# Performance work log

Hardware: AMD Instinct MI355X
Metric: run time of the kernel (lower is better)

## Reference

```python
import jax, jax.numpy as jnp
import numpy as np

B, S, E, H = 8, 1024, 1024, 16
D = E // H  # head dimension = 64


def setup_inputs() -> dict:
    key = jax.random.key(0)
    ks = jax.random.split(key, 9)
    sc = 1.0 / np.sqrt(E)
    return {
        "q": jax.random.normal(ks[0], (B, S, E), dtype=jnp.float32),
        "Wq_w": jax.random.normal(ks[1], (E, E), dtype=jnp.float32) * sc,
        "Wq_b": jax.random.normal(ks[2], (E,), dtype=jnp.float32) * 0.01,
        "Wk_w": jax.random.normal(ks[3], (E, E), dtype=jnp.float32) * sc,
        "Wk_b": jax.random.normal(ks[4], (E,), dtype=jnp.float32) * 0.01,
        "Wv_w": jax.random.normal(ks[5], (E, E), dtype=jnp.float32) * sc,
        "Wv_b": jax.random.normal(ks[6], (E,), dtype=jnp.float32) * 0.01,
        "Wo_w": jax.random.normal(ks[7], (E, E), dtype=jnp.float32) * sc,
        "Wo_b": jax.random.normal(ks[8], (E,), dtype=jnp.float32) * 0.01,
    }


def reference(q, Wq_w, Wq_b, Wk_w, Wk_b, Wv_w, Wv_b, Wo_w, Wo_b):
    # Linear projections (torch Linear: x @ W.T + b)
    Q = q @ Wq_w.T + Wq_b
    K = q @ Wk_w.T + Wk_b  # self-attention: k = v = q
    V = q @ Wv_w.T + Wv_b
    # [B, S, E] -> [B, H, S, D]
    Q = Q.reshape(B, S, H, D).transpose(0, 2, 1, 3)
    K = K.reshape(B, S, H, D).transpose(0, 2, 1, 3)
    V = V.reshape(B, S, H, D).transpose(0, 2, 1, 3)
    # Scores [B, H, S, S], scaled by sqrt(head_dim)
    scores = jnp.einsum('bhqd,bhkd->bhqk', Q, K) / jnp.sqrt(jnp.float32(D))
    attn = jax.nn.softmax(scores, axis=-1)
    # dropout p=0.0 (eval mode) -> identity
    out = jnp.einsum('bhqk,bhkd->bhqd', attn, V)
    out = out.transpose(0, 2, 1, 3).reshape(B, S, E)
    out = out @ Wo_w.T + Wo_b
    return out, attn
```

## Files before the change

### kernel.cpp

```cpp
#include <hip/hip_runtime.h>

using bf16x8 = __attribute__((ext_vector_type(8))) __bf16;
using f32x4  = __attribute__((ext_vector_type(4))) float;

#define NE 1024
#define C1E 0.18033688011112042f
#define C2E -11.541560327111707f

__device__ __forceinline__ unsigned short f2b(float f) {
    unsigned u = __builtin_bit_cast(unsigned, f);
    u = (u + 0x7FFFu + ((u >> 16) & 1u)) >> 16;
    return (unsigned short)u;
}

typedef __attribute__((address_space(1))) const void gvoid_t;
typedef __attribute__((address_space(3))) void lvoid_t;

__device__ __forceinline__ void stage128(const unsigned short* gbase, char* lds, int tid)
{
    const int w = tid >> 6, l = tid & 63;
    #pragma unroll
    for (int i = 0; i < 4; ++i) {
        int grp = i * 4 + w;
        int row = grp * 8 + (l >> 3);
        int srcb = ((l & 7) * 16) ^ ((l >> 3) << 4);
        const char* g = (const char*)(gbase + (size_t)row * NE) + srcb;
        char* d = lds + grp * 1024;
        __builtin_amdgcn_global_load_lds((gvoid_t*)g, (lvoid_t*)d, 16, 0, 0);
    }
}

__device__ __forceinline__ void stage64x256(const unsigned short* gbase, char* lds, int tid)
{
    const int w = tid >> 6, l = tid & 63;
    #pragma unroll
    for (int i = 0; i < 4; ++i) {
        int row0 = i * 16 + w * 4;
        int row = row0 + (l >> 4);
        int srcb = ((l & 15) * 16) ^ ((row & 7) << 4);
        const char* g = (const char*)(gbase + (size_t)row * 1024) + srcb;
        char* d = lds + row0 * 256;
        __builtin_amdgcn_global_load_lds((gvoid_t*)g, (lvoid_t*)d, 16, 0, 0);
    }
}

__global__ __launch_bounds__(256)
void conv_bf16(const float* __restrict__ src, unsigned short* __restrict__ dst)
{
    size_t i = ((size_t)blockIdx.x * 256 + threadIdx.x) * 8;
    float4 a0 = *(const float4*)(src + i);
    float4 a1 = *(const float4*)(src + i + 4);
    uint4 p;
    p.x = f2b(a0.x) | ((unsigned)f2b(a0.y) << 16);
    p.y = f2b(a0.z) | ((unsigned)f2b(a0.w) << 16);
    p.z = f2b(a1.x) | ((unsigned)f2b(a1.y) << 16);
    p.w = f2b(a1.z) | ((unsigned)f2b(a1.w) << 16);
    *(uint4*)(dst + i) = p;
}

template<int MODE>
__global__ __launch_bounds__(256)
void proj_bt(const unsigned short* __restrict__ A, const unsigned short* __restrict__ W,
             const float* __restrict__ bias, void* __restrict__ outp)
{
    __shared__ char Asm[16384], Bsm[16384];
    const int tid  = threadIdx.x;
    const int lane = tid & 63;
    const int wid  = tid >> 6;
    const int wr = wid >> 1, wc = wid & 1;
    const int swz = (blockIdx.x & 7) * 64 + (blockIdx.x >> 3);
    const int rowbase = (swz >> 3) * 128;
    const int colbase = (swz & 7) * 128;
    f32x4 acc[4][4] = {};

    for (int kt = 0; kt < 16; ++kt) {
        __syncthreads();
        stage128(A + (size_t)rowbase * NE + kt * 64, Asm, tid);
        stage128(W + (size_t)colbase * NE + kt * 64, Bsm, tid);
        __syncthreads();
        #pragma unroll
        for (int ks = 0; ks < 2; ++ks) {
            const int kb = ks * 64 + (lane >> 4) * 16;
            bf16x8 af[4], bf[4];
            #pragma unroll
            for (int m = 0; m < 4; ++m) {
                int row = wr * 64 + m * 16 + (lane & 15);
                af[m] = *(const bf16x8*)(Asm + ((row * 128 + kb) ^ ((row & 7) << 4)));
            }
            #pragma unroll
            for (int n = 0; n < 4; ++n) {
                int row = wc * 64 + n * 16 + (lane & 15);
                bf[n] = *(const bf16x8*)(Bsm + ((row * 128 + kb) ^ ((row & 7) << 4)));
            }
            #pragma unroll
            for (int m = 0; m < 4; ++m)
                #pragma unroll
                for (int n = 0; n < 4; ++n)
                    acc[m][n] = __builtin_amdgcn_mfma_f32_16x16x32_bf16(af[m], bf[n], acc[m][n], 0, 0, 0);
        }
    }

    #pragma unroll
    for (int m = 0; m < 4; ++m) {
        #pragma unroll
        for (int n = 0; n < 4; ++n) {
            int col = colbase + wc * 64 + n * 16 + (lane & 15);
            float bv = bias[col];
            #pragma unroll
            for (int r = 0; r < 4; ++r) {
                int row = rowbase + wr * 64 + m * 16 + (lane >> 4) * 4 + r;
                float v = acc[m][n][r] + bv;
                if (MODE == 0) {
                    ((unsigned short*)outp)[(size_t)row * NE + col] = f2b(v);
                } else if (MODE == 1) {
                    int b = row >> 10, s = row & 1023, h = col >> 6, d = col & 63;
                    ((unsigned short*)outp)[((size_t)((b * 16 + h) * 64 + d) << 10) + s] = f2b(v);
                } else {
                    ((float*)outp)[(size_t)row * NE + col] = v;
                }
            }
        }
    }
}

__global__ __launch_bounds__(256, 2)
void fused_attn(const unsigned short* __restrict__ Q,
                const unsigned short* __restrict__ K,
                const unsigned short* __restrict__ VT,
                float* __restrict__ attn, unsigned short* __restrict__ Og)
{
    __shared__ char Ksm[16384];
    __shared__ char Vsm[16384];
    __shared__ char Psm[32768];
    __shared__ float rs4[4][128];
    __shared__ float lt[128];
    const int tid  = threadIdx.x;
    const int lane = tid & 63;
    const int w    = tid >> 6;
    const int swzb = (blockIdx.x & 7) * 128 + (blockIdx.x >> 3);
    const int bh = swzb >> 3, qt = swzb & 7;
    const int b = bh >> 4, h = bh & 15;
    const unsigned short* Qg = Q  + (size_t)(b * 1024 + qt * 128) * 1024 + h * 64;
    const unsigned short* Kg = K  + (size_t)(b * 1024) * 1024 + h * 64;
    const unsigned short* Vg = VT + (size_t)bh * 64 * 1024;

    stage128(Qg, Psm, tid);
    __syncthreads();
    bf16x8 qf[2][8];
    #pragma unroll
    for (int ks = 0; ks < 2; ++ks) {
        const int kb = ks * 64 + (lane >> 4) * 16;
        #pragma unroll
        for (int n = 0; n < 8; ++n) {
            int row = n * 16 + (lane & 15);
            qf[ks][n] = *(const bf16x8*)(Psm + ((row * 128 + kb) ^ ((row & 7) << 4)));
        }
    }
    stage128(Kg, Ksm, tid);

    float rs_p[8] = {0.f, 0.f, 0.f, 0.f, 0.f, 0.f, 0.f, 0.f};
    for (int kt = 0; kt < 8; ++kt) {
        __syncthreads();
        f32x4 sa[2][8] = {};
        __builtin_amdgcn_s_setprio(1);
        #pragma unroll
        for (int ks = 0; ks < 2; ++ks) {
            const int kb = ks * 64 + (lane >> 4) * 16;
            bf16x8 kf[2];
            #pragma unroll
            for (int m = 0; m < 2; ++m) {
                int row = w * 32 + m * 16 + (lane & 15);
                kf[m] = *(const bf16x8*)(Ksm + ((row * 128 + kb) ^ ((row & 7) << 4)));
            }
            #pragma unroll
            for (int m = 0; m < 2; ++m)
                #pragma unroll
                for (int n = 0; n < 8; ++n)
                    sa[m][n] = __builtin_amdgcn_mfma_f32_16x16x32_bf16(kf[m], qf[ks][n], sa[m][n], 0, 0, 0);
        }
        __builtin_amdgcn_s_setprio(0);
        __syncthreads();
        if (kt < 7) stage128(Kg + (size_t)((kt + 1) * 128) * 1024, Ksm, tid);
        #pragma unroll
        for (int n = 0; n < 8; ++n)
            #pragma unroll
            for (int m = 0; m < 2; ++m)
                #pragma unroll
                for (int r = 0; r < 4; ++r)
                    rs_p[n] += exp2f(fmaf(sa[m][n][r], C1E, C2E));
    }
    #pragma unroll
    for (int n = 0; n < 8; ++n) {
        rs_p[n] += __shfl_xor(rs_p[n], 16);
        rs_p[n] += __shfl_xor(rs_p[n], 32);
    }
    if (lane < 16) {
        #pragma unroll
        for (int n = 0; n < 8; ++n) rs4[w][n * 16 + lane] = rs_p[n];
    }
    __syncthreads();
    if (tid < 128) {
        float l = rs4[0][tid] + rs4[1][tid] + rs4[2][tid] + rs4[3][tid];
        lt[tid] = C2E - __log2f(l);
    }
    stage128(Kg, Ksm, tid);

    f32x4 oa[2][4] = {};
    float* attnq = attn + ((size_t)bh * 1024 + qt * 128) * 1024;
    for (int kt = 0; kt < 8; ++kt) {
        __syncthreads();
        stage64x256(Vg + kt * 128, Vsm, tid);
        f32x4 sa[2][8] = {};
        __builtin_amdgcn_s_setprio(1);
        #pragma unroll
        for (int ks = 0; ks < 2; ++ks) {
            const int kb = ks * 64 + (lane >> 4) * 16;
            bf16x8 kf[2];
            #pragma unroll
            for (int m = 0; m < 2; ++m) {
                int row = w * 32 + m * 16 + (lane & 15);
                kf[m] = *(const bf16x8*)(Ksm + ((row * 128 + kb) ^ ((row & 7) << 4)));
            }
            #pragma unroll
            for (int m = 0; m < 2; ++m)
                #pragma unroll
                for (int n = 0; n < 8; ++n)
                    sa[m][n] = __builtin_amdgcn_mfma_f32_16x16x32_bf16(kf[m], qf[ks][n], sa[m][n], 0, 0, 0);
        }
        __builtin_amdgcn_s_setprio(0);
        #pragma unroll
        for (int n = 0; n < 8; ++n) {
            int q = n * 16 + (lane & 15);
            float ltq = lt[q];
            #pragma unroll
            for (int m = 0; m < 2; ++m) {
                int k0 = w * 32 + m * 16 + (lane >> 4) * 4;
                float4 p4;
                p4.x = exp2f(fmaf(sa[m][n][0], C1E, ltq));
                p4.y = exp2f(fmaf(sa[m][n][1], C1E, ltq));
                p4.z = exp2f(fmaf(sa[m][n][2], C1E, ltq));
                p4.w = exp2f(fmaf(sa[m][n][3], C1E, ltq));
                *(float4*)(attnq + (size_t)q * 1024 + kt * 128 + k0) = p4;
                uint2 pk;
                pk.x = f2b(p4.x) | ((unsigned)f2b(p4.y) << 16);
                pk.y = f2b(p4.z) | ((unsigned)f2b(p4.w) << 16);
                *(uint2*)(Psm + ((q * 256 + k0 * 2) ^ ((q & 7) << 4))) = pk;
            }
        }
        __syncthreads();
        if (kt < 7) stage128(Kg + (size_t)((kt + 1) * 128) * 1024, Ksm, tid);
        __builtin_amdgcn_s_setprio(1);
        #pragma unroll
        for (int ks = 0; ks < 4; ++ks) {
            const int kb = ks * 64 + (lane >> 4) * 16;
            bf16x8 pa[2], vb[4];
            #pragma unroll
            for (int m2 = 0; m2 < 2; ++m2) {
                int row = w * 32 + m2 * 16 + (lane & 15);
                pa[m2] = *(const bf16x8*)(Psm + ((row * 256 + kb) ^ ((row & 7) << 4)));
            }
            #pragma unroll
            for (int n2 = 0; n2 < 4; ++n2) {
                int d = n2 * 16 + (lane & 15);
                vb[n2] = *(const bf16x8*)(Vsm + d * 256 + (kb ^ ((d & 7) << 4)));
            }
            #pragma unroll
            for (int m2 = 0; m2 < 2; ++m2)
                #pragma unroll
                for (int n2 = 0; n2 < 4; ++n2)
                    oa[m2][n2] = __builtin_amdgcn_mfma_f32_16x16x32_bf16(pa[m2], vb[n2], oa[m2][n2], 0, 0, 0);
        }
        __builtin_amdgcn_s_setprio(0);
    }
    unsigned short* Ob = Og + (size_t)(b * 1024 + qt * 128) * 1024 + h * 64;
    #pragma unroll
    for (int m2 = 0; m2 < 2; ++m2)
        #pragma unroll
        for (int n2 = 0; n2 < 4; ++n2) {
            int d = n2 * 16 + (lane & 15);
            #pragma unroll
            for (int r = 0; r < 4; ++r) {
                int qrow = w * 32 + m2 * 16 + (lane >> 4) * 4 + r;
                Ob[(size_t)qrow * 1024 + d] = f2b(oa[m2][n2][r]);
            }
        }
}

extern "C" void kernel_launch(void* const* d_in, const int* in_sizes, int n_in,
                              void* d_out, int out_size, void* d_ws, size_t ws_size,
                              hipStream_t stream) {
    (void)in_sizes; (void)n_in; (void)out_size; (void)ws_size;
    const float* q    = (const float*)d_in[0];
    const float* Wq_w = (const float*)d_in[1];
    const float* Wq_b = (const float*)d_in[2];
    const float* Wk_w = (const float*)d_in[3];
    const float* Wk_b = (const float*)d_in[4];
    const float* Wv_w = (const float*)d_in[5];
    const float* Wv_b = (const float*)d_in[6];
    const float* Wo_w = (const float*)d_in[7];
    const float* Wo_b = (const float*)d_in[8];

    char* ws = (char*)d_ws;
    unsigned short* Qws  = (unsigned short*)(ws);
    unsigned short* Kws  = (unsigned short*)(ws + (16u << 20));
    unsigned short* VTws = (unsigned short*)(ws + (32u << 20));

    float* outp  = (float*)d_out;
    float* attnp = outp + 8388608;

    char* scr = (char*)attnp;
    unsigned short* qbf = (unsigned short*)scr;
    unsigned short* wqb = (unsigned short*)(scr + (16u << 20));
    unsigned short* wkb = (unsigned short*)(scr + (18u << 20));
    unsigned short* wvb = (unsigned short*)(scr + (20u << 20));

    dim3 blk(256);
    conv_bf16<<<dim3(4096), blk, 0, stream>>>(q, qbf);
    conv_bf16<<<dim3(512),  blk, 0, stream>>>(Wq_w, wqb);
    conv_bf16<<<dim3(512),  blk, 0, stream>>>(Wk_w, wkb);
    conv_bf16<<<dim3(512),  blk, 0, stream>>>(Wv_w, wvb);
    proj_bt<0><<<dim3(512), blk, 0, stream>>>(qbf, wqb, Wq_b, Qws);
    proj_bt<0><<<dim3(512), blk, 0, stream>>>(qbf, wkb, Wk_b, Kws);
    proj_bt<1><<<dim3(512), blk, 0, stream>>>(qbf, wvb, Wv_b, VTws);
    fused_attn<<<dim3(1024), blk, 0, stream>>>(Qws, Kws, VTws, attnp, Qws);
    conv_bf16<<<dim3(512),  blk, 0, stream>>>(Wo_w, Kws);
    proj_bt<2><<<dim3(512), blk, 0, stream>>>(Qws, Kws, Wo_b, outp);
}
```

Measured before the change: 287.5 us.

## Fuse QKV projections and conversions, single-pass attention with scores kept in registers

```diff
diff --git a/kernel.cpp b/kernel.cpp
--- a/kernel.cpp
+++ b/kernel.cpp
@@ -15,6 +15,7 @@
 
 typedef __attribute__((address_space(1))) const void gvoid_t;
 typedef __attribute__((address_space(3))) void lvoid_t;
+
 
 __device__ __forceinline__ void stage128(const unsigned short* gbase, char* lds, int tid)
 {
@@ -25,9 +26,30 @@
         int row = grp * 8 + (l >> 3);
         int srcb = ((l & 7) * 16) ^ ((l >> 3) << 4);
         const char* g = (const char*)(gbase + (size_t)row * NE) + srcb;
-        char* d = lds + grp * 1024;
-        __builtin_amdgcn_global_load_lds((gvoid_t*)g, (lvoid_t*)d, 16, 0, 0);
-    }
+        __builtin_amdgcn_global_load_lds((gvoid_t*)g, (lvoid_t*)(lds + grp * 1024), 16, 0, 0);
+    }
+}
+
+__device__ __forceinline__ void stage64x128(const unsigned short* gbase, char* lds, int tid)
+{
+    const int w = tid >> 6, l = tid & 63;
+    #pragma unroll
+    for (int i = 0; i < 2; ++i) {
+        int grp = i * 4 + w;
+        int row = grp * 8 + (l >> 3);
+        int srcb = ((l & 7) * 16) ^ ((l >> 3) << 4);
+        const char* g = (const char*)(gbase + (size_t)row * NE) + srcb;
+        __builtin_amdgcn_global_load_lds((gvoid_t*)g, (lvoid_t*)(lds + grp * 1024), 16, 0, 0);
+    }
+}
+
+__device__ __forceinline__ void stage32(const unsigned short* gbase, char* lds, int tid)
+{
+    const int w = tid >> 6, l = tid & 63;
+    int row = w * 8 + (l >> 3);
+    int srcb = ((l & 7) * 16) ^ ((l >> 3) << 4);
+    const char* g = (const char*)(gbase + (size_t)row * NE) + srcb;
+    __builtin_amdgcn_global_load_lds((gvoid_t*)g, (lvoid_t*)(lds + w * 1024), 16, 0, 0);
 }
 
 __device__ __forceinline__ void stage64x256(const unsigned short* gbase, char* lds, int tid)
@@ -39,8 +61,7 @@
         int row = row0 + (l >> 4);
         int srcb = ((l & 15) * 16) ^ ((row & 7) << 4);
         const char* g = (const char*)(gbase + (size_t)row * 1024) + srcb;
-        char* d = lds + row0 * 256;
-        __builtin_amdgcn_global_load_lds((gvoid_t*)g, (lvoid_t*)d, 16, 0, 0);
+        __builtin_amdgcn_global_load_lds((gvoid_t*)g, (lvoid_t*)(lds + row0 * 256), 16, 0, 0);
     }
 }
 
@@ -58,10 +79,104 @@
     *(uint4*)(dst + i) = p;
 }
 
-template<int MODE>
 __global__ __launch_bounds__(256)
-void proj_bt(const unsigned short* __restrict__ A, const unsigned short* __restrict__ W,
-             const float* __restrict__ bias, void* __restrict__ outp)
+void conv_all(const float* __restrict__ q, const float* __restrict__ w0,
+              const float* __restrict__ w1, const float* __restrict__ w2,
+              unsigned short* __restrict__ qd, unsigned short* __restrict__ d0,
+              unsigned short* __restrict__ d1, unsigned short* __restrict__ d2)
+{
+    int bid = blockIdx.x;
+    const float* s; unsigned short* d; size_t off;
+    if (bid < 4096) { s = q; d = qd; off = (size_t)bid * 2048; }
+    else {
+        int seg = (bid - 4096) >> 9, r = (bid - 4096) & 511;
+        s = seg == 0 ? w0 : (seg == 1 ? w1 : w2);
+        d = seg == 0 ? d0 : (seg == 1 ? d1 : d2);
+        off = (size_t)r * 2048;
+    }
+    size_t i = off + threadIdx.x * 8;
+    float4 a0 = *(const float4*)(s + i);
+    float4 a1 = *(const float4*)(s + i + 4);
+    uint4 p;
+    p.x = f2b(a0.x) | ((unsigned)f2b(a0.y) << 16);
+    p.y = f2b(a0.z) | ((unsigned)f2b(a0.w) << 16);
+    p.z = f2b(a1.x) | ((unsigned)f2b(a1.y) << 16);
+    p.w = f2b(a1.z) | ((unsigned)f2b(a1.w) << 16);
+    *(uint4*)(d + i) = p;
+}
+
+__global__ __launch_bounds__(256, 2)
+void qkv_proj(const unsigned short* __restrict__ A,
+              const unsigned short* __restrict__ Wq, const unsigned short* __restrict__ Wk,
+              const unsigned short* __restrict__ Wv,
+              const float* __restrict__ bq, const float* __restrict__ bk,
+              const float* __restrict__ bv,
+              unsigned short* __restrict__ Qo, unsigned short* __restrict__ Ko,
+              unsigned short* __restrict__ Vo)
+{
+    __shared__ char Asm[16384];
+    __shared__ char Bsm[3][8192];
+    const int tid  = threadIdx.x;
+    const int lane = tid & 63;
+    const int w    = tid >> 6;
+    const int swz = (blockIdx.x & 7) * 128 + (blockIdx.x >> 3);
+    const int rowbase = (swz >> 4) * 128;
+    const int colbase = (swz & 15) * 64;
+    f32x4 acc[3][2][4] = {};
+
+    for (int kt = 0; kt < 16; ++kt) {
+        __syncthreads();
+        stage128(A + (size_t)rowbase * NE + kt * 64, Asm, tid);
+        stage64x128(Wq + (size_t)colbase * NE + kt * 64, Bsm[0], tid);
+        stage64x128(Wk + (size_t)colbase * NE + kt * 64, Bsm[1], tid);
+        stage64x128(Wv + (size_t)colbase * NE + kt * 64, Bsm[2], tid);
+        __syncthreads();
+        #pragma unroll
+        for (int ks = 0; ks < 2; ++ks) {
+            const int kb = ks * 64 + (lane >> 4) * 16;
+            bf16x8 af[2], bf[3][4];
+            #pragma unroll
+            for (int m = 0; m < 2; ++m) {
+                int row = w * 32 + m * 16 + (lane & 15);
+                af[m] = *(const bf16x8*)(Asm + ((row * 128 + kb) ^ ((row & 7) << 4)));
+            }
+            #pragma unroll
+            for (int j = 0; j < 3; ++j)
+                #pragma unroll
+                for (int n = 0; n < 4; ++n) {
+                    int row = n * 16 + (lane & 15);
+                    bf[j][n] = *(const bf16x8*)(Bsm[j] + ((row * 128 + kb) ^ ((row & 7) << 4)));
+                }
+            #pragma unroll
+            for (int j = 0; j < 3; ++j)
+                #pragma unroll
+                for (int m = 0; m < 2; ++m)
+                    #pragma unroll
+                    for (int n = 0; n < 4; ++n)
+                        acc[j][m][n] = __builtin_amdgcn_mfma_f32_16x16x32_bf16(af[m], bf[j][n], acc[j][m][n], 0, 0, 0);
+        }
+    }
+
+    #pragma unroll
+    for (int m = 0; m < 2; ++m)
+        #pragma unroll
+        for (int n = 0; n < 4; ++n) {
+            int col = colbase + n * 16 + (lane & 15);
+            float bvq = bq[col], bvk = bk[col], bvv = bv[col];
+            #pragma unroll
+            for (int r = 0; r < 4; ++r) {
+                int row = rowbase + w * 32 + m * 16 + (lane >> 4) * 4 + r;
+                Qo[(size_t)row * NE + col] = f2b(acc[0][m][n][r] + bvq);
+                Ko[(size_t)row * NE + col] = f2b(acc[1][m][n][r] + bvk);
+                int b = row >> 10, s = row & 1023, h = col >> 6, d = col & 63;
+                Vo[((size_t)((b * 16 + h) * 64 + d) << 10) + s] = f2b(acc[2][m][n][r] + bvv);
+            }
+        }
+}
+
+__global__ __launch_bounds__(256)
+void proj_o(const unsigned short* __restrict__ A, const unsigned short* __restrict__ W,
+            const float* __restrict__ bias, float* __restrict__ outp)
 {
     __shared__ char Asm[16384], Bsm[16384];
     const int tid  = threadIdx.x;
@@ -101,7 +216,7 @@
     }
 
     #pragma unroll
-    for (int m = 0; m < 4; ++m) {
+    for (int m = 0; m < 4; ++m)
         #pragma unroll
         for (int n = 0; n < 4; ++n) {
             int col = colbase + wc * 64 + n * 16 + (lane & 15);
@@ -109,18 +224,9 @@
             #pragma unroll
             for (int r = 0; r < 4; ++r) {
                 int row = rowbase + wr * 64 + m * 16 + (lane >> 4) * 4 + r;
-                float v = acc[m][n][r] + bv;
-                if (MODE == 0) {
-                    ((unsigned short*)outp)[(size_t)row * NE + col] = f2b(v);
-                } else if (MODE == 1) {
-                    int b = row >> 10, s = row & 1023, h = col >> 6, d = col & 63;
-                    ((unsigned short*)outp)[((size_t)((b * 16 + h) * 64 + d) << 10) + s] = f2b(v);
-                } else {
-                    ((float*)outp)[(size_t)row * NE + col] = v;
-                }
-            }
-        }
-    }
+                outp[(size_t)row * NE + col] = acc[m][n][r] + bv;
+            }
+        }
 }
 
 __global__ __launch_bounds__(256, 2)
@@ -130,38 +236,38 @@
                 float* __restrict__ attn, unsigned short* __restrict__ Og)
 {
     __shared__ char Ksm[16384];
-    __shared__ char Vsm[16384];
-    __shared__ char Psm[32768];
-    __shared__ float rs4[4][128];
-    __shared__ float lt[128];
+    __shared__ char Vsm[2][16384];
+    __shared__ char Psm[8192];
+    __shared__ float rs4[4][32];
+    __shared__ float il[32];
     const int tid  = threadIdx.x;
     const int lane = tid & 63;
     const int w    = tid >> 6;
-    const int swzb = (blockIdx.x & 7) * 128 + (blockIdx.x >> 3);
-    const int bh = swzb >> 3, qt = swzb & 7;
+    const int swzb = (blockIdx.x & 7) * 512 + (blockIdx.x >> 3);
+    const int bh = swzb >> 5, qt = swzb & 31;
     const int b = bh >> 4, h = bh & 15;
-    const unsigned short* Qg = Q  + (size_t)(b * 1024 + qt * 128) * 1024 + h * 64;
+    const unsigned short* Qg = Q  + (size_t)(b * 1024 + qt * 32) * 1024 + h * 64;
     const unsigned short* Kg = K  + (size_t)(b * 1024) * 1024 + h * 64;
     const unsigned short* Vg = VT + (size_t)bh * 64 * 1024;
 
-    stage128(Qg, Psm, tid);
+    stage32(Qg, Psm, tid);
+    stage128(Kg, Ksm, tid);
     __syncthreads();
-    bf16x8 qf[2][8];
+    bf16x8 qf[2][2];
     #pragma unroll
     for (int ks = 0; ks < 2; ++ks) {
         const int kb = ks * 64 + (lane >> 4) * 16;
         #pragma unroll
-        for (int n = 0; n < 8; ++n) {
+        for (int n = 0; n < 2; ++n) {
             int row = n * 16 + (lane & 15);
             qf[ks][n] = *(const bf16x8*)(Psm + ((row * 128 + kb) ^ ((row & 7) << 4)));
         }
     }
-    stage128(Kg, Ksm, tid);
-
-    float rs_p[8] = {0.f, 0.f, 0.f, 0.f, 0.f, 0.f, 0.f, 0.f};
+
+    f32x4 sacc[8][2][2] = {};
+    float rs_p[2] = {0.f, 0.f};
+    #pragma unroll
     for (int kt = 0; kt < 8; ++kt) {
-        __syncthreads();
-        f32x4 sa[2][8] = {};
         __builtin_amdgcn_s_setprio(1);
         #pragma unroll
         for (int ks = 0; ks < 2; ++ks) {
@@ -175,71 +281,55 @@
             #pragma unroll
             for (int m = 0; m < 2; ++m)
                 #pragma unroll
-                for (int n = 0; n < 8; ++n)
-                    sa[m][n] = __builtin_amdgcn_mfma_f32_16x16x32_bf16(kf[m], qf[ks][n], sa[m][n], 0, 0, 0);
+                for (int n = 0; n < 2; ++n)
+                    sacc[kt][m][n] = __builtin_amdgcn_mfma_f32_16x16x32_bf16(kf[m], qf[ks][n], sacc[kt][m][n], 0, 0, 0);
         }
         __builtin_amdgcn_s_setprio(0);
         __syncthreads();
         if (kt < 7) stage128(Kg + (size_t)((kt + 1) * 128) * 1024, Ksm, tid);
-        #pragma unroll
-        for (int n = 0; n < 8; ++n)
-            #pragma unroll
-            for (int m = 0; m < 2; ++m)
+        else        stage64x256(Vg, Vsm[0], tid);
+        #pragma unroll
+        for (int m = 0; m < 2; ++m)
+            #pragma unroll
+            for (int n = 0; n < 2; ++n)
                 #pragma unroll
-                for (int r = 0; r < 4; ++r)
-                    rs_p[n] += exp2f(fmaf(sa[m][n][r], C1E, C2E));
-    }
-    #pragma unroll
-    for (int n = 0; n < 8; ++n) {
+                for (int r = 0; r < 4; ++r) {
+                    float e = exp2f(fmaf(sacc[kt][m][n][r], C1E, C2E));
+                    sacc[kt][m][n][r] = e;
+                    rs_p[n] += e;
+                }
+        __syncthreads();
+    }
+
+    #pragma unroll
+    for (int n = 0; n < 2; ++n) {
         rs_p[n] += __shfl_xor(rs_p[n], 16);
         rs_p[n] += __shfl_xor(rs_p[n], 32);
     }
     if (lane < 16) {
-        #pragma unroll
-        for (int n = 0; n < 8; ++n) rs4[w][n * 16 + lane] = rs_p[n];
+        rs4[w][lane]      = rs_p[0];
+        rs4[w][16 + lane] = rs_p[1];
     }
     __syncthreads();
-    if (tid < 128) {
-        float l = rs4[0][tid] + rs4[1][tid] + rs4[2][tid] + rs4[3][tid];
-        lt[tid] = C2E - __log2f(l);
-    }
-    stage128(Kg, Ksm, tid);
-
-    f32x4 oa[2][4] = {};
-    float* attnq = attn + ((size_t)bh * 1024 + qt * 128) * 1024;
+    if (tid < 32) il[tid] = 1.0f / (rs4[0][tid] + rs4[1][tid] + rs4[2][tid] + rs4[3][tid]);
+    __syncthreads();
+
+    f32x4 oa[2] = {};
+    float* attnq = attn + ((size_t)bh * 1024 + qt * 32) * 1024;
+    #pragma unroll
     for (int kt = 0; kt < 8; ++kt) {
-        __syncthreads();
-        stage64x256(Vg + kt * 128, Vsm, tid);
-        f32x4 sa[2][8] = {};
-        __builtin_amdgcn_s_setprio(1);
-        #pragma unroll
-        for (int ks = 0; ks < 2; ++ks) {
-            const int kb = ks * 64 + (lane >> 4) * 16;
-            bf16x8 kf[2];
-            #pragma unroll
-            for (int m = 0; m < 2; ++m) {
-                int row = w * 32 + m * 16 + (lane & 15);
-                kf[m] = *(const bf16x8*)(Ksm + ((row * 128 + kb) ^ ((row & 7) << 4)));
-            }
-            #pragma unroll
-            for (int m = 0; m < 2; ++m)
-                #pragma unroll
-                for (int n = 0; n < 8; ++n)
-                    sa[m][n] = __builtin_amdgcn_mfma_f32_16x16x32_bf16(kf[m], qf[ks][n], sa[m][n], 0, 0, 0);
-        }
-        __builtin_amdgcn_s_setprio(0);
-        #pragma unroll
-        for (int n = 0; n < 8; ++n) {
+        #pragma unroll
+        for (int n = 0; n < 2; ++n) {
             int q = n * 16 + (lane & 15);
-            float ltq = lt[q];
+            float iv = il[q];
             #pragma unroll
             for (int m = 0; m < 2; ++m) {
                 int k0 = w * 32 + m * 16 + (lane >> 4) * 4;
                 float4 p4;
-                p4.x = exp2f(fmaf(sa[m][n][0], C1E, ltq));
-                p4.y = exp2f(fmaf(sa[m][n][1], C1E, ltq));
-                p4.z = exp2f(fmaf(sa[m][n][2], C1E, ltq));
-                p4.w = exp2f(fmaf(sa[m][n][3], C1E, ltq));
+                p4.x = sacc[kt][m][n][0] * iv;
+                p4.y = sacc[kt][m][n][1] * iv;
+                p4.z = sacc[kt][m][n][2] * iv;
+                p4.w = sacc[kt][m][n][3] * iv;
                 *(float4*)(attnq + (size_t)q * 1024 + kt * 128 + k0) = p4;
                 uint2 pk;
                 pk.x = f2b(p4.x) | ((unsigned)f2b(p4.y) << 16);
@@ -248,42 +338,39 @@
             }
         }
         __syncthreads();
-        if (kt < 7) stage128(Kg + (size_t)((kt + 1) * 128) * 1024, Ksm, tid);
+        if (kt < 7) stage64x256(Vg + (kt + 1) * 128, Vsm[(kt + 1) & 1], tid);
         __builtin_amdgcn_s_setprio(1);
         #pragma unroll
         for (int ks = 0; ks < 4; ++ks) {
             const int kb = ks * 64 + (lane >> 4) * 16;
-            bf16x8 pa[2], vb[4];
+            bf16x8 pa[2], vb;
             #pragma unroll
             for (int m2 = 0; m2 < 2; ++m2) {
-                int row = w * 32 + m2 * 16 + (lane & 15);
+                int row = m2 * 16 + (lane & 15);
                 pa[m2] = *(const bf16x8*)(Psm + ((row * 256 + kb) ^ ((row & 7) << 4)));
             }
-            #pragma unroll
-            for (int n2 = 0; n2 < 4; ++n2) {
-                int d = n2 * 16 + (lane & 15);
-                vb[n2] = *(const bf16x8*)(Vsm + d * 256 + (kb ^ ((d & 7) << 4)));
+            {
+                int d = w * 16 + (lane & 15);
+                vb = *(const bf16x8*)(Vsm[kt & 1] + d * 256 + (kb ^ ((d & 7) << 4)));
             }
             #pragma unroll
             for (int m2 = 0; m2 < 2; ++m2)
-                #pragma unroll
-                for (int n2 = 0; n2 < 4; ++n2)
-                    oa[m2][n2] = __builtin_amdgcn_mfma_f32_16x16x32_bf16(pa[m2], vb[n2], oa[m2][n2], 0, 0, 0);
+                oa[m2] = __builtin_amdgcn_mfma_f32_16x16x32_bf16(pa[m2], vb, oa[m2], 0, 0, 0);
         }
         __builtin_amdgcn_s_setprio(0);
-    }
-    unsigned short* Ob = Og + (size_t)(b * 1024 + qt * 128) * 1024 + h * 64;
-    #pragma unroll
-    for (int m2 = 0; m2 < 2; ++m2)
-        #pragma unroll
-        for (int n2 = 0; n2 < 4; ++n2) {
-            int d = n2 * 16 + (lane & 15);
-            #pragma unroll
-            for (int r = 0; r < 4; ++r) {
-                int qrow = w * 32 + m2 * 16 + (lane >> 4) * 4 + r;
-                Ob[(size_t)qrow * 1024 + d] = f2b(oa[m2][n2][r]);
-            }
-        }
+        __syncthreads();
+    }
+
+    unsigned short* Ob = Og + (size_t)(b * 1024 + qt * 32) * 1024 + h * 64;
+    #pragma unroll
+    for (int m2 = 0; m2 < 2; ++m2) {
+        int d = w * 16 + (lane & 15);
+        #pragma unroll
+        for (int r = 0; r < 4; ++r) {
+            int qrow = m2 * 16 + (lane >> 4) * 4 + r;
+            Ob[(size_t)qrow * 1024 + d] = f2b(oa[m2][r]);
+        }
+    }
 }
 
 extern "C" void kernel_launch(void* const* d_in, const int* in_sizes, int n_in,
@@ -315,14 +402,9 @@
     unsigned short* wvb = (unsigned short*)(scr + (20u << 20));
 
     dim3 blk(256);
-    conv_bf16<<<dim3(4096), blk, 0, stream>>>(q, qbf);
-    conv_bf16<<<dim3(512),  blk, 0, stream>>>(Wq_w, wqb);
-    conv_bf16<<<dim3(512),  blk, 0, stream>>>(Wk_w, wkb);
-    conv_bf16<<<dim3(512),  blk, 0, stream>>>(Wv_w, wvb);
-    proj_bt<0><<<dim3(512), blk, 0, stream>>>(qbf, wqb, Wq_b, Qws);
-    proj_bt<0><<<dim3(512), blk, 0, stream>>>(qbf, wkb, Wk_b, Kws);
-    proj_bt<1><<<dim3(512), blk, 0, stream>>>(qbf, wvb, Wv_b, VTws);
-    fused_attn<<<dim3(1024), blk, 0, stream>>>(Qws, Kws, VTws, attnp, Qws);
-    conv_bf16<<<dim3(512),  blk, 0, stream>>>(Wo_w, Kws);
-    proj_bt<2><<<dim3(512), blk, 0, stream>>>(Qws, Kws, Wo_b, outp);
-}
+    conv_all<<<dim3(4096 + 3 * 512), blk, 0, stream>>>(q, Wq_w, Wk_w, Wv_w, qbf, wqb, wkb, wvb);
+    qkv_proj<<<dim3(1024), blk, 0, stream>>>(qbf, wqb, wkb, wvb, Wq_b, Wk_b, Wv_b, Qws, Kws, VTws);
+    fused_attn<<<dim3(4096), blk, 0, stream>>>(Qws, Kws, VTws, attnp, Qws);
+    conv_bf16<<<dim3(512), blk, 0, stream>>>(Wo_w, Kws);
+    proj_o<<<dim3(512), blk, 0, stream>>>(Qws, Kws, Wo_b, outp);
+}
```

New measurement: 344.2 us. 1.2x slower.
